# Performance work log

Hardware: AMD Instinct MI355X
Metric: run time of the kernel (lower is better)

Reference implementation:

```python
import jax, jax.numpy as jnp
import numpy as np

ALPHA = 0.25
GAMMA = 2.0
OBJ_POS_WEIGHT = 1.5
CLS_W, REG_W, OBJ_W = 2.5, 5.0, 0.5
B, M, C, IMG = 64, 50, 4, 1280


def setup_inputs() -> dict:
    key = jax.random.key(0)
    ks = jax.random.split(key, 12)
    shapes = {
        'cls_p3': (B, C, 160, 160), 'reg_p3': (B, 4, 160, 160), 'obj_p3': (B, 1, 160, 160),
        'cls_p4': (B, C, 80, 80),   'reg_p4': (B, 4, 80, 80),   'obj_p4': (B, 1, 80, 80),
        'cls_p5': (B, C, 40, 40),   'reg_p5': (B, 4, 40, 40),   'obj_p5': (B, 1, 40, 40),
    }
    inp = {name: jax.random.normal(k, s, dtype=jnp.float32)
           for (name, s), k in zip(shapes.items(), ks[:9])}
    # boxes in pixel xyxy: sample two corners uniformly, sort so x2>=x1, y2>=y1
    raw = jax.random.uniform(ks[9], (B, M, 4), dtype=jnp.float32) * IMG
    x1 = jnp.minimum(raw[..., 0], raw[..., 2]); x2 = jnp.maximum(raw[..., 0], raw[..., 2])
    y1 = jnp.minimum(raw[..., 1], raw[..., 3]); y2 = jnp.maximum(raw[..., 1], raw[..., 3])
    inp['boxes'] = jnp.stack([x1, y1, x2, y2], axis=-1)
    inp['labels'] = jax.random.randint(ks[10], (B, M), 0, C, dtype=jnp.int32)
    inp['box_valid'] = jax.random.randint(ks[11], (B, M), 0, 2, dtype=jnp.int32)
    inp['img_size'] = IMG
    return inp


def _bce_logits(x, t):
    # numerically stable BCE-with-logits, elementwise
    return jnp.maximum(x, 0.0) - x * t + jnp.log1p(jnp.exp(-jnp.abs(x)))


def _focal(x, t):
    bce = _bce_logits(x, t)
    p = jax.nn.sigmoid(x)
    p_t = p * t + (1.0 - p) * (1.0 - t)
    a_w = ALPHA * t + (1.0 - ALPHA) * (1.0 - t)
    return jnp.mean(a_w * (1.0 - p_t) ** GAMMA * bce)


def _smooth_l1(d):
    a = jnp.abs(d)
    return jnp.where(a < 1.0, 0.5 * d * d, a - 0.5)


def _build_targets(boxes, labels, valid, stride, Bn, Cn, H, W):
    cx = (boxes[..., 0] + boxes[..., 2]) * 0.5 / stride  # [B,M]
    cy = (boxes[..., 1] + boxes[..., 3]) * 0.5 / stride
    gx = jnp.clip(cx.astype(jnp.int32), 0, W - 1)
    gy = jnp.clip(cy.astype(jnp.int32), 0, H - 1)
    gy_s = jnp.where(valid > 0, gy, H)  # invalid boxes -> out of bounds -> dropped
    b = jnp.broadcast_to(jnp.arange(Bn)[:, None], gx.shape)
    w = jnp.maximum(boxes[..., 2] - boxes[..., 0], 1.0)
    h = jnp.maximum(boxes[..., 3] - boxes[..., 1], 1.0)
    vals = jnp.stack([cx - gx.astype(cx.dtype), cy - gy.astype(cy.dtype),
                      jnp.log(w / stride), jnp.log(h / stride)], axis=-1)  # [B,M,4]
    cls_t = jnp.zeros((Bn, Cn, H, W), jnp.float32).at[b, labels, gy_s, gx].set(1.0, mode='drop')
    obj_t = jnp.zeros((Bn, 1, H, W), jnp.float32).at[b, 0, gy_s, gx].set(1.0, mode='drop')
    ch = jnp.arange(4)
    reg_t = jnp.zeros((Bn, 4, H, W), jnp.float32).at[
        b[:, :, None], ch[None, None, :], gy_s[:, :, None], gx[:, :, None]].set(vals, mode='drop')
    mask = jnp.zeros((Bn, 1, H, W), jnp.float32).at[b, 0, gy_s, gx].set(1.0, mode='drop')
    return cls_t, reg_t, obj_t, mask


def _detection_loss(scales, boxes, labels, valid):
    total_cls = jnp.float32(0.0); total_reg = jnp.float32(0.0); total_obj = jnp.float32(0.0)
    for (cls_p, reg_p, obj_p, stride) in scales:
        Bn, Cn, H, W = cls_p.shape
        cls_t, reg_t, obj_t, mask = _build_targets(boxes, labels, valid, stride, Bn, Cn, H, W)
        total_cls = total_cls + _focal(cls_p, cls_t)
        # BCEWithLogits with pos_weight on positives, mean reduction
        obj_bce = -(OBJ_POS_WEIGHT * obj_t * jax.nn.log_sigmoid(obj_p)
                    + (1.0 - obj_t) * jax.nn.log_sigmoid(-obj_p))
        total_obj = total_obj + jnp.mean(obj_bce)
        mask4 = jnp.broadcast_to(mask, reg_p.shape)
        denom = jnp.sum(mask4)
        reg_l = jnp.sum(_smooth_l1(reg_p - reg_t) * mask4) / jnp.maximum(denom, 1.0)
        total_reg = total_reg + jnp.where(denom > 0, reg_l, 0.0)
    total = CLS_W * total_cls + REG_W * total_reg + OBJ_W * total_obj
    return total, total_cls, total_reg, total_obj


def reference(cls_p3, reg_p3, obj_p3, cls_p4, reg_p4, obj_p4, cls_p5, reg_p5, obj_p5,
              boxes, labels, box_valid, img_size):
    scales = [(cls_p3, reg_p3, obj_p3, 8.0),
              (cls_p4, reg_p4, obj_p4, 16.0),
              (cls_p5, reg_p5, obj_p5, 32.0)]
    return _detection_loss(scales, boxes, labels, box_valid)
```

## Files before the change

### kernel.cpp

```cpp
#include <hip/hip_runtime.h>
#include <math.h>

static constexpr int Bn = 64, Mn = 50, Cn = 4;
static constexpr int CORR_BLOCKS = 64;
static constexpr int DENSE_BLOCKS = 512;
static constexpr int TOTAL_BLOCKS = CORR_BLOCKS + DENSE_BLOCKS;

static constexpr int BASE_OFF = 12 * 64;

typedef float floatx4 __attribute__((ext_vector_type(4)));

#define LOG2E 1.4426950408889634f
#define LN2   0.6931471805599453f

__device__ __forceinline__ float frcp (float x){ return __builtin_amdgcn_rcpf(x); }
__device__ __forceinline__ float fexp2(float x){ return __builtin_amdgcn_exp2f(x); }
__device__ __forceinline__ float flog2(float x){ return __builtin_amdgcn_logf(x); }

__device__ __forceinline__ float proc4(floatx4 v, float cf) {
  float s = 0.f;
#pragma unroll
  for (int k = 0; k < 4; ++k) {
    float x = v[k];
    float e   = fexp2(-LOG2E * fabsf(x));
    float ope = 1.f + e;
    float u   = frcp(ope);
    float sp  = fmaxf(x, 0.f) + LN2 * flog2(ope);
    float p   = (x >= 0.f) ? u : (1.f - u);
    float w   = fmaf(cf, fmaf(0.75f, p * p, -1.f), 1.f);
    s = fmaf(sp, w, s);
  }
  return s;
}

__device__ __forceinline__ float wave_reduce(float v) {
#pragma unroll
  for (int off = 32; off > 0; off >>= 1) v += __shfl_down(v, off, 64);
  return v;
}

__global__ __launch_bounds__(1024, 8) void main_kernel(
    const float* __restrict__ cls3, const float* __restrict__ reg3, const float* __restrict__ obj3,
    const float* __restrict__ cls4, const float* __restrict__ reg4, const float* __restrict__ obj4,
    const float* __restrict__ cls5, const float* __restrict__ reg5, const float* __restrict__ obj5,
    const float* __restrict__ boxes, const int* __restrict__ labels, const int* __restrict__ valid,
    float* __restrict__ ws) {
  if (blockIdx.x < CORR_BLOCKS) {
    __shared__ int s_cell[3][Mn];
    __shared__ int s_lab[Mn];
    __shared__ float cacc[12];

    const int b = blockIdx.x;
    const int tid = threadIdx.x;
    if (tid < 12) cacc[tid] = 0.f;

    const int s = tid / Mn;
    const int m = tid - s * Mn;

    float x1 = 0.f, y1 = 0.f, x2 = 0.f, y2 = 0.f;
    int lab = 0, val = 0;
    float cx = 0.f, cy = 0.f, strf = 8.f;
    int gx = 0, gy = 0, cell = -1, W = 160;

    if (tid < 150) {
      const float* bp = boxes + ((size_t)b * Mn + m) * 4;
      x1 = bp[0]; y1 = bp[1]; x2 = bp[2]; y2 = bp[3];
      lab = labels[b * Mn + m];
      val = valid[b * Mn + m];
      if (s == 0) s_lab[m] = lab;

      W = 160 >> s;
      strf = (float)(8 << s);
      if (val > 0) {
        float inv_s = frcp(strf);
        cx = (x1 + x2) * 0.5f * inv_s;
        cy = (y1 + y2) * 0.5f * inv_s;
        gx = min(max((int)cx, 0), W - 1);
        gy = min(max((int)cy, 0), W - 1);
        cell = gy * W + gx;
      }
      s_cell[s][m] = cell;
    }
    __syncthreads();

    if (tid < 150 && cell >= 0) {
      const float* clsP = (s == 0) ? cls3 : ((s == 1) ? cls4 : cls5);
      const float* regP = (s == 0) ? reg3 : ((s == 1) ? reg4 : reg5);
      const float* objP = (s == 0) ? obj3 : ((s == 1) ? obj4 : obj5);

      bool firstObj = true, lastReg = true, firstCls = true;
      for (int j = 0; j < Mn; ++j) {
        if (j == m) continue;
        if (s_cell[s][j] != cell) continue;
        if (j < m) {
          firstObj = false;
          if (s_lab[j] == lab) firstCls = false;
        } else {
          lastReg = false;
        }
      }
      size_t plane = (size_t)W * W;
      size_t pix = (size_t)gy * W + gx;

      if (firstObj) {
        float x = objP[(size_t)b * plane + pix];
        float e = fexp2(-LOG2E * fabsf(x));
        float sp = fmaxf(x, 0.f) + LN2 * flog2(1.f + e);
        float corr = 0.5f * sp - 1.5f * x;
        atomicAdd(&cacc[3 + s], corr);
        atomicAdd(&cacc[9 + s], 4.0f);
      }
      if (firstCls) {
        float x = clsP[((size_t)b * Cn + lab) * plane + pix];
        float e = fexp2(-LOG2E * fabsf(x));
        float ope = 1.f + e;
        float u = frcp(ope);
        float sp = fmaxf(x, 0.f) + LN2 * flog2(ope);
        float spn = sp - x;
        float p2 = (x >= 0.f) ? u : (1.f - u);
        float q = 1.f - p2;
        float corr = 0.25f * q * q * spn - 0.75f * p2 * p2 * sp;
        atomicAdd(&cacc[0 + s], corr);
      }
      if (lastReg) {
        float w = fmaxf(x2 - x1, 1.f), h = fmaxf(y2 - y1, 1.f);
        float inv_s = frcp(strf);
        float t0 = cx - (float)gx, t1 = cy - (float)gy;
        float t2 = LN2 * flog2(w * inv_s), t3 = LN2 * flog2(h * inv_s);
        const float* rp = regP + (size_t)b * 4 * plane + pix;
        float sum = 0.f, dd, a;
        dd = rp[0]         - t0; a = fabsf(dd); sum += (a < 1.f) ? 0.5f * dd * dd : a - 0.5f;
        dd = rp[plane]     - t1; a = fabsf(dd); sum += (a < 1.f) ? 0.5f * dd * dd : a - 0.5f;
        dd = rp[2 * plane] - t2; a = fabsf(dd); sum += (a < 1.f) ? 0.5f * dd * dd : a - 0.5f;
        dd = rp[3 * plane] - t3; a = fabsf(dd); sum += (a < 1.f) ? 0.5f * dd * dd : a - 0.5f;
        atomicAdd(&cacc[6 + s], sum);
      }
    }
    __syncthreads();
    if (tid < 12) ws[tid * 64 + b] = cacc[tid];
  } else {
    __shared__ float sdata[16];
    const int d = (int)blockIdx.x - CORR_BLOCKS;
    const int tid = threadIdx.x;

    const floatx4* sb; int bk, nB, nT; float cf;
    if (d < 311)      { sb = (const floatx4*)cls3; bk = d;       nB = 311; nT = 1600; cf = 1.f; }
    else if (d < 389) { sb = (const floatx4*)cls4; bk = d - 311; nB = 78;  nT = 400;  cf = 1.f; }
    else if (d < 409) { sb = (const floatx4*)cls5; bk = d - 389; nB = 20;  nT = 100;  cf = 1.f; }
    else if (d < 487) { sb = (const floatx4*)obj3; bk = d - 409; nB = 78;  nT = 400;  cf = 0.f; }
    else if (d < 507) { sb = (const floatx4*)obj4; bk = d - 487; nB = 20;  nT = 100;  cf = 0.f; }
    else              { sb = (const floatx4*)obj5; bk = d - 507; nB = 5;   nT = 25;   cf = 0.f; }

    float s = 0.f;
    int t = bk;
    floatx4 v = __builtin_nontemporal_load(&sb[(size_t)t * 1024 + tid]);
    for (t += nB; t < nT; t += nB) {
      floatx4 vn = __builtin_nontemporal_load(&sb[(size_t)t * 1024 + tid]);
      s += proc4(v, cf);
      v = vn;
    }
    s += proc4(v, cf);

    s = wave_reduce(s);
    const int lane = tid & 63;
    const int wid = tid >> 6;
    if (lane == 0) sdata[wid] = s;
    __syncthreads();
    if (tid == 0) {
      float r = 0.f;
#pragma unroll
      for (int i = 0; i < 16; ++i) r += sdata[i];
      ws[BASE_OFF + d] = r;
    }
  }
}

__global__ __launch_bounds__(256) void finalize_kernel(
    const float* __restrict__ ws, float* __restrict__ out) {
  __shared__ float sdata[6][4];
  __shared__ float res[18];
  const int t = threadIdx.x;
  const int lane = t & 63;
  const int wid = t >> 6;

  float a0 = 0.f, a1 = 0.f, a2 = 0.f, a3 = 0.f, a4 = 0.f, a5 = 0.f;
  for (int i = t; i < DENSE_BLOCKS; i += 256) {
    float v = ws[BASE_OFF + i];
    if (i < 311)      a0 += v;
    else if (i < 389) a1 += v;
    else if (i < 409) a2 += v;
    else if (i < 487) a3 += v;
    else if (i < 507) a4 += v;
    else              a5 += v;
  }
  float acc[6] = {a0, a1, a2, a3, a4, a5};
#pragma unroll
  for (int k = 0; k < 6; ++k) {
    float s = wave_reduce(acc[k]);
    if (lane == 0) sdata[k][wid] = s;
  }
  __syncthreads();
  if (t < 6) res[t] = sdata[t][0] + sdata[t][1] + sdata[t][2] + sdata[t][3];

  if (wid == 0) {
#pragma unroll
    for (int j = 0; j < 12; ++j) {
      float v = ws[j * 64 + lane];
      v = wave_reduce(v);
      if (lane == 0) res[6 + j] = v;
    }
  }
  __syncthreads();

  if (t == 0) {
    const float cls_cnt[3] = {6553600.f, 1638400.f, 409600.f};
    const float obj_cnt[3] = {1638400.f, 409600.f, 102400.f};
    float tc = 0.f, to = 0.f, tr = 0.f;
#pragma unroll
    for (int s = 0; s < 3; ++s) {
      tc += (res[s] + res[6 + s]) / cls_cnt[s];
      to += (res[3 + s] + res[9 + s]) / obj_cnt[s];
      float den = res[15 + s];
      if (den > 0.f) tr += res[12 + s] / fmaxf(den, 1.f);
    }
    float total = 2.5f * tc + 5.0f * tr + 0.5f * to;
    out[0] = total; out[1] = tc; out[2] = tr; out[3] = to;
  }
}

extern "C" void kernel_launch(void* const* d_in, const int* in_sizes, int n_in,
                              void* d_out, int out_size, void* d_ws, size_t ws_size,
                              hipStream_t stream) {
  const float* cls3 = (const float*)d_in[0];
  const float* reg3 = (const float*)d_in[1];
  const float* obj3 = (const float*)d_in[2];
  const float* cls4 = (const float*)d_in[3];
  const float* reg4 = (const float*)d_in[4];
  const float* obj4 = (const float*)d_in[5];
  const float* cls5 = (const float*)d_in[6];
  const float* reg5 = (const float*)d_in[7];
  const float* obj5 = (const float*)d_in[8];
  const float* boxes = (const float*)d_in[9];
  const int* labels = (const int*)d_in[10];
  const int* valid = (const int*)d_in[11];
  float* ws = (float*)d_ws;
  float* out = (float*)d_out;

  main_kernel<<<TOTAL_BLOCKS, 1024, 0, stream>>>(
      cls3, reg3, obj3, cls4, reg4, obj4, cls5, reg5, obj5,
      boxes, labels, valid, ws);

  finalize_kernel<<<1, 256, 0, stream>>>(ws, out);
}
```

Before: 23.12 us.

## Fuse finalize into main kernel via last-block atomic counter

Drops the separate finalize launch. Each block increments a global counter after writing its partial sums, and the last block to arrive does the final reduction using agent-scope loads. A hipMemsetAsync resets the counter before each launch. This removes one kernel launch and the gap between launches, at the cost of a memset node plus a fence and atomic in every block.

New measurement: 49.27 us. 2.13x slower.

```diff
diff --git a/kernel.cpp b/kernel.cpp
--- a/kernel.cpp
+++ b/kernel.cpp
@@ -7,6 +7,7 @@
 static constexpr int TOTAL_BLOCKS = CORR_BLOCKS + DENSE_BLOCKS;
 
 static constexpr int BASE_OFF = 12 * 64;
+static constexpr int CNT_OFF  = 1280;
 
 typedef float floatx4 __attribute__((ext_vector_type(4)));
 
@@ -16,6 +17,10 @@
 __device__ __forceinline__ float frcp (float x){ return __builtin_amdgcn_rcpf(x); }
 __device__ __forceinline__ float fexp2(float x){ return __builtin_amdgcn_exp2f(x); }
 __device__ __forceinline__ float flog2(float x){ return __builtin_amdgcn_logf(x); }
+
+__device__ __forceinline__ float agent_load(const float* p) {
+  return __hip_atomic_load(p, __ATOMIC_RELAXED, __HIP_MEMORY_SCOPE_AGENT);
+}
 
 __device__ __forceinline__ float proc4(floatx4 v, float cf) {
   float s = 0.f;
@@ -44,14 +49,16 @@
     const float* __restrict__ cls4, const float* __restrict__ reg4, const float* __restrict__ obj4,
     const float* __restrict__ cls5, const float* __restrict__ reg5, const float* __restrict__ obj5,
     const float* __restrict__ boxes, const int* __restrict__ labels, const int* __restrict__ valid,
-    float* __restrict__ ws) {
+    float* __restrict__ ws, float* __restrict__ out) {
+  __shared__ int slast;
+  const int tid = threadIdx.x;
+
   if (blockIdx.x < CORR_BLOCKS) {
     __shared__ int s_cell[3][Mn];
     __shared__ int s_lab[Mn];
     __shared__ float cacc[12];
 
     const int b = blockIdx.x;
-    const int tid = threadIdx.x;
     if (tid < 12) cacc[tid] = 0.f;
 
     const int s = tid / Mn;
@@ -141,7 +148,6 @@
   } else {
     __shared__ float sdata[16];
     const int d = (int)blockIdx.x - CORR_BLOCKS;
-    const int tid = threadIdx.x;
 
     const floatx4* sb; int bk, nB, nT; float cf;
     if (d < 311)      { sb = (const floatx4*)cls3; bk = d;       nB = 311; nT = 1600; cf = 1.f; }
@@ -173,46 +179,56 @@
       ws[BASE_OFF + d] = r;
     }
   }
-}
-
-__global__ __launch_bounds__(256) void finalize_kernel(
-    const float* __restrict__ ws, float* __restrict__ out) {
-  __shared__ float sdata[6][4];
+
+  __syncthreads();
+  if (tid == 0) {
+    __threadfence();
+    unsigned old = atomicAdd((unsigned*)&ws[CNT_OFF], 1u);
+    slast = (old == (unsigned)(TOTAL_BLOCKS - 1)) ? 1 : 0;
+  }
+  __syncthreads();
+  if (!slast) return;
+
+  __shared__ float sd[6][16];
   __shared__ float res[18];
-  const int t = threadIdx.x;
-  const int lane = t & 63;
-  const int wid = t >> 6;
+  const int lane = tid & 63;
+  const int wid = tid >> 6;
+  __threadfence();
 
   float a0 = 0.f, a1 = 0.f, a2 = 0.f, a3 = 0.f, a4 = 0.f, a5 = 0.f;
-  for (int i = t; i < DENSE_BLOCKS; i += 256) {
-    float v = ws[BASE_OFF + i];
-    if (i < 311)      a0 += v;
-    else if (i < 389) a1 += v;
-    else if (i < 409) a2 += v;
-    else if (i < 487) a3 += v;
-    else if (i < 507) a4 += v;
-    else              a5 += v;
-  }
-  float acc[6] = {a0, a1, a2, a3, a4, a5};
-#pragma unroll
-  for (int k = 0; k < 6; ++k) {
-    float s = wave_reduce(acc[k]);
-    if (lane == 0) sdata[k][wid] = s;
-  }
-  __syncthreads();
-  if (t < 6) res[t] = sdata[t][0] + sdata[t][1] + sdata[t][2] + sdata[t][3];
-
-  if (wid == 0) {
+  if (tid < DENSE_BLOCKS) {
+    float v = agent_load(&ws[BASE_OFF + tid]);
+    if (tid < 311)      a0 = v;
+    else if (tid < 389) a1 = v;
+    else if (tid < 409) a2 = v;
+    else if (tid < 487) a3 = v;
+    else if (tid < 507) a4 = v;
+    else                a5 = v;
+  }
+  a0 = wave_reduce(a0); a1 = wave_reduce(a1); a2 = wave_reduce(a2);
+  a3 = wave_reduce(a3); a4 = wave_reduce(a4); a5 = wave_reduce(a5);
+  if (lane == 0) {
+    sd[0][wid] = a0; sd[1][wid] = a1; sd[2][wid] = a2;
+    sd[3][wid] = a3; sd[4][wid] = a4; sd[5][wid] = a5;
+  }
+  if (wid == 1) {
 #pragma unroll
     for (int j = 0; j < 12; ++j) {
-      float v = ws[j * 64 + lane];
+      float v = agent_load(&ws[j * 64 + lane]);
       v = wave_reduce(v);
       if (lane == 0) res[6 + j] = v;
     }
   }
   __syncthreads();
-
-  if (t == 0) {
+  if (tid < 6) {
+    float r = 0.f;
+#pragma unroll
+    for (int i = 0; i < 16; ++i) r += sd[tid][i];
+    res[tid] = r;
+  }
+  __syncthreads();
+
+  if (tid == 0) {
     const float cls_cnt[3] = {6553600.f, 1638400.f, 409600.f};
     const float obj_cnt[3] = {1638400.f, 409600.f, 102400.f};
     float tc = 0.f, to = 0.f, tr = 0.f;
@@ -246,9 +262,9 @@
   float* ws = (float*)d_ws;
   float* out = (float*)d_out;
 
+  hipMemsetAsync((char*)d_ws + CNT_OFF * sizeof(float), 0, 4, stream);
+
   main_kernel<<<TOTAL_BLOCKS, 1024, 0, stream>>>(
       cls3, reg3, obj3, cls4, reg4, obj4, cls5, reg5, obj5,
-      boxes, labels, valid, ws);
-
-  finalize_kernel<<<1, 256, 0, stream>>>(ws, out);
-}
+      boxes, labels, valid, ws, out);
+}
```
